# Kernel tuning notes

Hardware: AMD Instinct MI355X
Metric: run time of the kernel (lower is better)

## Reference

```python
import jax, jax.numpy as jnp
import numpy as np

ENC_DIM = 1024
DEC_DIM = 1024
BATCH = 32
SRC_LEN = 2048


def setup_inputs() -> dict:
    key = jax.random.key(0)
    k1, k2, k3, k4, k5 = jax.random.split(key, 5)
    hidden = jax.random.normal(k1, (BATCH, DEC_DIM), dtype=jnp.float32)
    encoder_outputs = jax.random.normal(k2, (SRC_LEN, BATCH, ENC_DIM), dtype=jnp.float32)
    # nn.Linear(enc+dec, dec): weight [dec, enc+dec], bias [dec]
    fan_in = ENC_DIM + DEC_DIM
    bound = 1.0 / np.sqrt(fan_in)
    attn_w = jax.random.uniform(k3, (DEC_DIM, fan_in), dtype=jnp.float32, minval=-bound, maxval=bound)
    attn_b = jax.random.uniform(k4, (DEC_DIM,), dtype=jnp.float32, minval=-bound, maxval=bound)
    # self.v = nn.Parameter(torch.rand(dec)) -> uniform [0,1)
    v = jax.random.uniform(k5, (DEC_DIM,), dtype=jnp.float32)
    return {"hidden": hidden, "encoder_outputs": encoder_outputs,
            "attn_w": attn_w, "attn_b": attn_b, "v": v}


def reference(hidden, encoder_outputs, attn_w, attn_b, v):
    src_len, batch, _ = encoder_outputs.shape
    # hidden.repeat(src_len,1,1): [src_len, batch, dec]
    h = jnp.broadcast_to(hidden[None, :, :], (src_len, batch, hidden.shape[-1]))
    x = jnp.concatenate([h, encoder_outputs], axis=2)  # [S, B, enc+dec]
    energy = jnp.tanh(jnp.einsum('sbf,df->sbd', x, attn_w) + attn_b)  # [S, B, dec]
    # v-weighted reduction over dec dim -> scores [B, S]
    scores = jnp.einsum('sbd,d->bs', energy, v)
    return jax.nn.softmax(scores, axis=1)
```

## Files before the change

kernel.cpp:

```cpp
#include <hip/hip_runtime.h>
#include <hip/hip_bf16.h>

typedef __bf16 bf16x8 __attribute__((ext_vector_type(8)));
typedef __bf16 bf16x4 __attribute__((ext_vector_type(4)));
typedef float f32x4 __attribute__((ext_vector_type(4)));

#define S_LEN 2048
#define BATCH 32
#define DIM   1024
#define FAN   (2*DIM)

__device__ __forceinline__ unsigned short f2bf(float f) {
    union { float f; unsigned u; } x; x.f = f;
    unsigned r = x.u + 0x7FFFu + ((x.u >> 16) & 1u);
    return (unsigned short)(r >> 16);
}

__device__ __forceinline__ float fast_tanh(float x) {
    float e = __expf(2.0f * x);
    return 1.0f - 2.0f / (e + 1.0f);
}

__device__ __forceinline__ int swz(int row, int col) {
    return row * 128 + (col ^ ((row & 7) << 4));
}

__device__ __forceinline__ void gload16(const void* g, void* l) {
    __builtin_amdgcn_global_load_lds((const __attribute__((address_space(1))) void*)g,
                                     (__attribute__((address_space(3))) void*)l, 16, 0, 0);
}

__global__ __launch_bounds__(256) void k_prep(const float* __restrict__ enc,
                                              unsigned short* __restrict__ encbf,
                                              const float* __restrict__ attn_w,
                                              unsigned short* __restrict__ w2bf,
                                              const float* __restrict__ hidden,
                                              const float* __restrict__ attn_b,
                                              float* __restrict__ hw) {
    const int bid = blockIdx.x, tid = threadIdx.x;
    if (bid < 4096) {
        const size_t stride = (size_t)4096 * 256;
        const size_t n8 = (size_t)S_LEN * BATCH * DIM / 8;
        for (size_t i = (size_t)bid * 256 + tid; i < n8; i += stride) {
            float4 a = ((const float4*)enc)[2 * i];
            float4 b = ((const float4*)enc)[2 * i + 1];
            bf16x8 o;
            o[0] = (__bf16)a.x; o[1] = (__bf16)a.y; o[2] = (__bf16)a.z; o[3] = (__bf16)a.w;
            o[4] = (__bf16)b.x; o[5] = (__bf16)b.y; o[6] = (__bf16)b.z; o[7] = (__bf16)b.w;
            ((bf16x8*)encbf)[i] = o;
        }
    } else if (bid < 5120) {
        const int t = (bid - 4096) * 256 + tid;
        const int n  = t >> 8;
        const int k4 = (t & 255) * 4;
        float4 w = *(const float4*)(attn_w + (size_t)n * FAN + DIM + k4);
        ushort4 o;
        o.x = f2bf(w.x); o.y = f2bf(w.y); o.z = f2bf(w.z); o.w = f2bf(w.w);
        *(ushort4*)(w2bf + (size_t)n * DIM + k4) = o;
    } else {
        const int d = bid - 5120;
        const int lane = tid & 63, w = tid >> 6;
        const float* wrow = attn_w + (size_t)d * FAN + lane * 4;
        float4 wv[4];
        #pragma unroll
        for (int c = 0; c < 4; ++c) wv[c] = *(const float4*)(wrow + c * 256);
        const float bd = attn_b[d];
        #pragma unroll
        for (int bb = 0; bb < 8; ++bb) {
            const int b = w * 8 + bb;
            const float* hrow = hidden + (size_t)b * DIM + lane * 4;
            float s = 0.f;
            #pragma unroll
            for (int c = 0; c < 4; ++c) {
                float4 h = *(const float4*)(hrow + c * 256);
                s += wv[c].x*h.x + wv[c].y*h.y + wv[c].z*h.z + wv[c].w*h.w;
            }
            #pragma unroll
            for (int o = 32; o; o >>= 1) s += __shfl_xor(s, o);
            if (lane == 0) hw[(size_t)b * DIM + d] = s + bd;
        }
    }
}

__global__ __launch_bounds__(256, 4) void k_main(const unsigned short* __restrict__ encbf,
                                                 const unsigned short* __restrict__ w2bf,
                                                 const float* __restrict__ hw,
                                                 const float* __restrict__ vvec,
                                                 float* __restrict__ partials) {
    __shared__ unsigned char Asm[128 * 128];
    __shared__ unsigned char Bsm[128 * 128];
    const int tid = threadIdx.x;

    const int x  = blockIdx.x & 7;
    const int ii = blockIdx.x >> 3;
    const int nb = ii & 7;
    const int mb = ((ii >> 3) << 3) | x;
    const int m0 = mb * 128, n0 = nb * 128;
    const int lane = tid & 63, wid = tid >> 6;
    const int wr = wid >> 1, wc = wid & 1;

    const int row8 = lane >> 3, colx = (lane & 7) ^ row8;
    const unsigned short* asrc[4];
    const unsigned short* bsrc[4];
    #pragma unroll
    for (int p = 0; p < 4; ++p) {
        const int c = wid * 4 + p;
        asrc[p] = encbf + (size_t)(m0 + 8 * c + row8) * DIM + colx * 8;
        bsrc[p] = w2bf  + (size_t)(n0 + 8 * c + row8) * DIM + colx * 8;
    }

    f32x4 acc[4][4];
    #pragma unroll
    for (int i2 = 0; i2 < 4; ++i2)
        #pragma unroll
        for (int j = 0; j < 4; ++j) acc[i2][j] = (f32x4){0.f, 0.f, 0.f, 0.f};

    #pragma unroll 1
    for (int t = 0; t < 16; ++t) {
        __syncthreads();
        #pragma unroll
        for (int p = 0; p < 4; ++p) {
            gload16(asrc[p] + t * 64, (void*)&Asm[(wid * 4 + p) * 1024]);
            gload16(bsrc[p] + t * 64, (void*)&Bsm[(wid * 4 + p) * 1024]);
        }
        __syncthreads();

        const int lrow = lane & 15;
        const int kbyte0 = (lane >> 4) * 16;
        #pragma unroll
        for (int kk = 0; kk < 2; ++kk) {
            const int kbyte = kbyte0 + kk * 64;
            bf16x8 af[4], bfr[4];
            #pragma unroll
            for (int i2 = 0; i2 < 4; ++i2)
                af[i2] = *(const bf16x8*)(&Asm[swz(wr * 64 + i2 * 16 + lrow, kbyte)]);
            #pragma unroll
            for (int j = 0; j < 4; ++j)
                bfr[j] = *(const bf16x8*)(&Bsm[swz(wc * 64 + j * 16 + lrow, kbyte)]);
            #pragma unroll
            for (int i2 = 0; i2 < 4; ++i2)
                #pragma unroll
                for (int j = 0; j < 4; ++j)
                    acc[i2][j] = __builtin_amdgcn_mfma_f32_16x16x32_bf16(af[i2], bfr[j], acc[i2][j], 0, 0, 0);
        }
    }

    const int colg = lane & 15, rowg = lane >> 4;
    #pragma unroll
    for (int i2 = 0; i2 < 4; ++i2) {
        #pragma unroll
        for (int r = 0; r < 4; ++r) {
            const int m = m0 + wr * 64 + i2 * 16 + rowg * 4 + r;
            const float* hwrow = hw + (size_t)(m & 31) * DIM + n0 + wc * 64;
            const float* vrow  = vvec + n0 + wc * 64;
            float sumv = 0.f;
            #pragma unroll
            for (int j = 0; j < 4; ++j) {
                const int nl = j * 16 + colg;
                float pre = acc[i2][j][r] + hwrow[nl];
                sumv += vrow[nl] * fast_tanh(pre);
            }
            sumv += __shfl_xor(sumv, 1);
            sumv += __shfl_xor(sumv, 2);
            sumv += __shfl_xor(sumv, 4);
            sumv += __shfl_xor(sumv, 8);
            if (colg == 0) partials[(size_t)m * 16 + nb * 2 + wc] = sumv;
        }
    }
}

__global__ __launch_bounds__(256) void k_main_f32(const float* __restrict__ enc,
                                                  const unsigned short* __restrict__ w2bf,
                                                  const float* __restrict__ hw,
                                                  const float* __restrict__ vvec,
                                                  float* __restrict__ partials) {
    __shared__ unsigned char Asm[128 * 128];
    __shared__ unsigned char Bsm[2][128 * 128];
    const int tid = threadIdx.x;
    const int x  = blockIdx.x & 7;
    const int ii = blockIdx.x >> 3;
    const int nb = ii & 7;
    const int mb = ((ii >> 3) << 3) | x;
    const int m0 = mb * 128, n0 = nb * 128;
    const int lane = tid & 63, wid = tid >> 6;
    const int wr = wid >> 1, wc = wid & 1;
    const int ar = tid >> 4, ac = tid & 15;
    const float* aptr = enc + (size_t)(m0 + ar) * DIM + ac * 4;
    const int row8 = lane >> 3, colx = (lane & 7) ^ row8;
    const unsigned short* bsrc[4];
    #pragma unroll
    for (int p = 0; p < 4; ++p)
        bsrc[p] = w2bf + (size_t)(n0 + 8 * (wid * 4 + p) + row8) * DIM + colx * 8;

    f32x4 acc[4][4];
    #pragma unroll
    for (int i2 = 0; i2 < 4; ++i2)
        #pragma unroll
        for (int j = 0; j < 4; ++j) acc[i2][j] = (f32x4){0.f, 0.f, 0.f, 0.f};

    float4 areg[8];
    #pragma unroll
    for (int p = 0; p < 8; ++p) areg[p] = *(const float4*)(aptr + p * 16 * DIM);
    #pragma unroll
    for (int p = 0; p < 4; ++p)
        gload16(bsrc[p], (void*)&Bsm[0][(wid * 4 + p) * 1024]);

    #pragma unroll 1
    for (int t = 0; t < 16; ++t) {
        asm volatile("s_waitcnt lgkmcnt(0)" ::: "memory");
        __builtin_amdgcn_s_barrier();
        #pragma unroll
        for (int p = 0; p < 8; ++p) {
            bf16x4 c;
            c[0] = (__bf16)areg[p].x; c[1] = (__bf16)areg[p].y;
            c[2] = (__bf16)areg[p].z; c[3] = (__bf16)areg[p].w;
            *(bf16x4*)(&Asm[swz(ar + p * 16, ac * 8)]) = c;
        }
        if (t + 1 < 16) {
            const int ko = (t + 1) * 64;
            #pragma unroll
            for (int p = 0; p < 8; ++p) areg[p] = *(const float4*)(aptr + ko + p * 16 * DIM);
            #pragma unroll
            for (int p = 0; p < 4; ++p)
                gload16(bsrc[p] + (size_t)(t + 1) * 64,
                        (void*)&Bsm[(t + 1) & 1][(wid * 4 + p) * 1024]);
            asm volatile("s_waitcnt vmcnt(12)" ::: "memory");
        } else {
            asm volatile("s_waitcnt vmcnt(0)" ::: "memory");
        }
        asm volatile("s_waitcnt lgkmcnt(0)" ::: "memory");
        __builtin_amdgcn_s_barrier();

        const unsigned char* bbase = &Bsm[t & 1][0];
        const int lrow = lane & 15;
        const int kbyte0 = (lane >> 4) * 16;
        #pragma unroll
        for (int kk = 0; kk < 2; ++kk) {
            const int kbyte = kbyte0 + kk * 64;
            bf16x8 af[4], bfr[4];
            #pragma unroll
            for (int i2 = 0; i2 < 4; ++i2)
                af[i2] = *(const bf16x8*)(&Asm[swz(wr * 64 + i2 * 16 + lrow, kbyte)]);
            #pragma unroll
            for (int j = 0; j < 4; ++j)
                bfr[j] = *(const bf16x8*)(&bbase[swz(wc * 64 + j * 16 + lrow, kbyte)]);
            #pragma unroll
            for (int i2 = 0; i2 < 4; ++i2)
                #pragma unroll
                for (int j = 0; j < 4; ++j)
                    acc[i2][j] = __builtin_amdgcn_mfma_f32_16x16x32_bf16(af[i2], bfr[j], acc[i2][j], 0, 0, 0);
        }
    }

    const int colg = lane & 15, rowg = lane >> 4;
    #pragma unroll
    for (int i2 = 0; i2 < 4; ++i2) {
        #pragma unroll
        for (int r = 0; r < 4; ++r) {
            const int m = m0 + wr * 64 + i2 * 16 + rowg * 4 + r;
            const float* hwrow = hw + (size_t)(m & 31) * DIM + n0 + wc * 64;
            const float* vrow  = vvec + n0 + wc * 64;
            float sumv = 0.f;
            #pragma unroll
            for (int j = 0; j < 4; ++j) {
                const int nl = j * 16 + colg;
                float pre = acc[i2][j][r] + hwrow[nl];
                sumv += vrow[nl] * fast_tanh(pre);
            }
            sumv += __shfl_xor(sumv, 1);
            sumv += __shfl_xor(sumv, 2);
            sumv += __shfl_xor(sumv, 4);
            sumv += __shfl_xor(sumv, 8);
            if (colg == 0) partials[(size_t)m * 16 + nb * 2 + wc] = sumv;
        }
    }
}

__global__ __launch_bounds__(1024) void k_softmax(const float* __restrict__ partials,
                                                  float* __restrict__ out) {
    const int b = blockIdx.x;
    const int tid = threadIdx.x;
    __shared__ float redm[16], reds[16];
    float loc[2];
    float mx = -1e30f;
    #pragma unroll
    for (int i = 0; i < 2; ++i) {
        const int s = tid + i * 1024;
        const float4* p = (const float4*)(partials + ((size_t)s * 32 + b) * 16);
        float4 p0 = p[0], p1 = p[1], p2 = p[2], p3 = p[3];
        float v = ((p0.x + p0.y) + (p0.z + p0.w)) + ((p1.x + p1.y) + (p1.z + p1.w))
                + ((p2.x + p2.y) + (p2.z + p2.w)) + ((p3.x + p3.y) + (p3.z + p3.w));
        loc[i] = v; mx = fmaxf(mx, v);
    }
    #pragma unroll
    for (int o = 32; o; o >>= 1) mx = fmaxf(mx, __shfl_xor(mx, o));
    const int wid2 = tid >> 6, lane = tid & 63;
    if (lane == 0) redm[wid2] = mx;
    __syncthreads();
    mx = redm[0];
    #pragma unroll
    for (int w = 1; w < 16; ++w) mx = fmaxf(mx, redm[w]);
    float sum = 0.f;
    #pragma unroll
    for (int i = 0; i < 2; ++i) { float e = __expf(loc[i] - mx); loc[i] = e; sum += e; }
    #pragma unroll
    for (int o = 32; o; o >>= 1) sum += __shfl_xor(sum, o);
    if (lane == 0) reds[wid2] = sum;
    __syncthreads();
    sum = 0.f;
    #pragma unroll
    for (int w = 0; w < 16; ++w) sum += reds[w];
    const float rs = 1.0f / sum;
    #pragma unroll
    for (int i = 0; i < 2; ++i) out[(size_t)b * S_LEN + tid + i * 1024] = loc[i] * rs;
}

extern "C" void kernel_launch(void* const* d_in, const int* in_sizes, int n_in,
                              void* d_out, int out_size, void* d_ws, size_t ws_size,
                              hipStream_t stream) {
    const float* hidden = (const float*)d_in[0];
    const float* enc    = (const float*)d_in[1];
    const float* attn_w = (const float*)d_in[2];
    const float* attn_b = (const float*)d_in[3];
    const float* v      = (const float*)d_in[4];
    float* out = (float*)d_out;

    char* ws = (char*)d_ws;
    float*          hw       = (float*)ws;
    unsigned short* w2bf     = (unsigned short*)(ws + (128u << 10));
    float*          partials = (float*)(ws + (128u << 10) + (2u << 20));
    unsigned short* encbf    = (unsigned short*)(ws + (128u << 10) + (6u << 20));
    const size_t NEED = (128u << 10) + (6u << 20) + ((size_t)S_LEN * BATCH * DIM * 2);

    if (ws_size >= NEED) {
        hipLaunchKernelGGL(k_prep, dim3(6144), dim3(256), 0, stream,
                           enc, encbf, attn_w, w2bf, hidden, attn_b, hw);
        hipLaunchKernelGGL(k_main, dim3(4096), dim3(256), 0, stream, encbf, w2bf, hw, v, partials);
    } else {
        hipLaunchKernelGGL(k_prep, dim3(6144), dim3(256), 0, stream,
                           enc, (unsigned short*)w2bf , attn_w, w2bf, hidden, attn_b, hw);
        hipLaunchKernelGGL(k_main_f32, dim3(4096), dim3(256), 0, stream, enc, w2bf, hw, v, partials);
    }
    hipLaunchKernelGGL(k_softmax, dim3(32), dim3(1024), 0, stream, partials, out);
}
```

Measured before the change: 244.1 us.

## Replace 128x128 GEMM with 256x256 eight-wave ping-pong pipelined kernel

The main bf16 GEMM kernel is replaced by a 512-thread kernel computing 256x256 output tiles with double-buffered LDS in quadrants. Global loads for future k-steps are issued inside eight interleaved compute phases, with barriers and setprio around the MFMA bursts, so memory traffic overlaps matrix math. Larger tiles halve the operand reloads per output and cut the block count to 1024. The cost is 128KB of LDS per block and heavier register pressure, which limits occupancy to about one or two blocks per CU.

Measured after the change: 264.4 us. +8.3%, slower.

```diff
diff --git a/kernel.cpp b/kernel.cpp
--- a/kernel.cpp
+++ b/kernel.cpp
@@ -82,91 +82,137 @@
     }
 }
 
-__global__ __launch_bounds__(256, 4) void k_main(const unsigned short* __restrict__ encbf,
-                                                 const unsigned short* __restrict__ w2bf,
-                                                 const float* __restrict__ hw,
-                                                 const float* __restrict__ vvec,
-                                                 float* __restrict__ partials) {
-    __shared__ unsigned char Asm[128 * 128];
-    __shared__ unsigned char Bsm[128 * 128];
+#define ASLOT(PAR,HH) (((PAR)*2+(HH)) << 14)
+
+#define STAGE_A(tt, HH, PAR) do {                                                    \
+    gload16(aSb[HH][0] + (tt) * 64, (void*)&Asm[ASLOT(PAR,HH) + ((wid*2+0) << 10)]); \
+    gload16(aSb[HH][1] + (tt) * 64, (void*)&Asm[ASLOT(PAR,HH) + ((wid*2+1) << 10)]); \
+  } while (0)
+
+#define STAGE_B(tt, HH, PAR) do {                                                    \
+    gload16(bSb[HH][0] + (tt) * 64, (void*)&Bsm[ASLOT(PAR,HH) + ((wid*2+0) << 10)]); \
+    gload16(bSb[HH][1] + (tt) * 64, (void*)&Bsm[ASLOT(PAR,HH) + ((wid*2+1) << 10)]); \
+  } while (0)
+
+#define PHASE(PAR, MQ, NQ, LA, LB, STAGE_STMT, VMCNT_STMT)                           \
+  {                                                                                  \
+    if (LA) {                                                                        \
+      _Pragma("unroll") for (int i2 = 0; i2 < 4; ++i2)                               \
+      _Pragma("unroll") for (int kk = 0; kk < 2; ++kk)                               \
+        afr[i2][kk] = *(const bf16x8*)(&Asm[ASLOT(PAR,MQ) +                          \
+                         swz(wr * 64 + i2 * 16 + lrow, kk * 64 + khb)]);             \
+    }                                                                                \
+    if (LB) {                                                                        \
+      _Pragma("unroll") for (int j = 0; j < 2; ++j)                                  \
+      _Pragma("unroll") for (int kk = 0; kk < 2; ++kk)                               \
+        bfr[j][kk] = *(const bf16x8*)(&Bsm[ASLOT(PAR,NQ) +                           \
+                         swz(wc * 32 + j * 16 + lrow, kk * 64 + khb)]);              \
+    }                                                                                \
+    STAGE_STMT;                                                                      \
+    VMCNT_STMT;                                                                      \
+    __builtin_amdgcn_s_barrier();                                                    \
+    asm volatile("s_waitcnt lgkmcnt(0)" ::: "memory");                               \
+    __builtin_amdgcn_sched_barrier(0);                                               \
+    __builtin_amdgcn_s_setprio(1);                                                   \
+    _Pragma("unroll") for (int i2 = 0; i2 < 4; ++i2)                                 \
+    _Pragma("unroll") for (int j = 0; j < 2; ++j)                                    \
+    _Pragma("unroll") for (int kk = 0; kk < 2; ++kk)                                 \
+      acc[MQ][NQ][i2][j] = __builtin_amdgcn_mfma_f32_16x16x32_bf16(                  \
+          afr[i2][kk], bfr[j][kk], acc[MQ][NQ][i2][j], 0, 0, 0);                     \
+    __builtin_amdgcn_s_setprio(0);                                                   \
+    __builtin_amdgcn_sched_barrier(0);                                               \
+    __builtin_amdgcn_s_barrier();                                                    \
+  }
+
+__global__ __launch_bounds__(512, 2) void k_main8(const unsigned short* __restrict__ encbf,
+                                                  const unsigned short* __restrict__ w2bf,
+                                                  const float* __restrict__ hw,
+                                                  const float* __restrict__ vvec,
+                                                  float* __restrict__ partials) {
+    __shared__ unsigned char Asm[4 * 16384];
+    __shared__ unsigned char Bsm[4 * 16384];
     const int tid = threadIdx.x;
 
     const int x  = blockIdx.x & 7;
     const int ii = blockIdx.x >> 3;
-    const int nb = ii & 7;
-    const int mb = ((ii >> 3) << 3) | x;
-    const int m0 = mb * 128, n0 = nb * 128;
+    const int nb = ii & 3;
+    const int mb = (ii >> 2) * 8 + x;
+    const int m0 = mb * 256, n0 = nb * 256;
     const int lane = tid & 63, wid = tid >> 6;
-    const int wr = wid >> 1, wc = wid & 1;
+    const int wr = wid >> 2, wc = wid & 3;
+    const int lrow = lane & 15, khb = (lane >> 4) * 16;
 
     const int row8 = lane >> 3, colx = (lane & 7) ^ row8;
-    const unsigned short* asrc[4];
-    const unsigned short* bsrc[4];
-    #pragma unroll
-    for (int p = 0; p < 4; ++p) {
-        const int c = wid * 4 + p;
-        asrc[p] = encbf + (size_t)(m0 + 8 * c + row8) * DIM + colx * 8;
-        bsrc[p] = w2bf  + (size_t)(n0 + 8 * c + row8) * DIM + colx * 8;
-    }
-
-    f32x4 acc[4][4];
-    #pragma unroll
-    for (int i2 = 0; i2 < 4; ++i2)
-        #pragma unroll
-        for (int j = 0; j < 4; ++j) acc[i2][j] = (f32x4){0.f, 0.f, 0.f, 0.f};
+    const unsigned short* aSb[2][2];
+    const unsigned short* bSb[2][2];
+    #pragma unroll
+    for (int h = 0; h < 2; ++h)
+        #pragma unroll
+        for (int q = 0; q < 2; ++q) {
+            aSb[h][q] = encbf + (size_t)(m0 + h * 128 + 16 * wid + 8 * q + row8) * DIM + colx * 8;
+            bSb[h][q] = w2bf  + (size_t)(n0 + h * 128 + 16 * wid + 8 * q + row8) * DIM + colx * 8;
+        }
+
+    f32x4 acc[2][2][4][2];
+    #pragma unroll
+    for (int a = 0; a < 2; ++a)
+        #pragma unroll
+        for (int b = 0; b < 2; ++b)
+            #pragma unroll
+            for (int c = 0; c < 4; ++c)
+                #pragma unroll
+                for (int d = 0; d < 2; ++d) acc[a][b][c][d] = (f32x4){0.f, 0.f, 0.f, 0.f};
+
+    bf16x8 afr[4][2], bfr[2][2];
+
+    STAGE_A(0, 0, 0);
+    STAGE_A(0, 1, 0);
+    STAGE_B(0, 0, 0);
+    STAGE_B(0, 1, 0);
+    STAGE_A(1, 0, 1);
+    STAGE_B(1, 1, 1);
+    asm volatile("s_waitcnt vmcnt(4)" ::: "memory");
+    __builtin_amdgcn_s_barrier();
 
     #pragma unroll 1
-    for (int t = 0; t < 16; ++t) {
-        __syncthreads();
-        #pragma unroll
-        for (int p = 0; p < 4; ++p) {
-            gload16(asrc[p] + t * 64, (void*)&Asm[(wid * 4 + p) * 1024]);
-            gload16(bsrc[p] + t * 64, (void*)&Bsm[(wid * 4 + p) * 1024]);
-        }
-        __syncthreads();
-
-        const int lrow = lane & 15;
-        const int kbyte0 = (lane >> 4) * 16;
-        #pragma unroll
-        for (int kk = 0; kk < 2; ++kk) {
-            const int kbyte = kbyte0 + kk * 64;
-            bf16x8 af[4], bfr[4];
-            #pragma unroll
-            for (int i2 = 0; i2 < 4; ++i2)
-                af[i2] = *(const bf16x8*)(&Asm[swz(wr * 64 + i2 * 16 + lrow, kbyte)]);
-            #pragma unroll
-            for (int j = 0; j < 4; ++j)
-                bfr[j] = *(const bf16x8*)(&Bsm[swz(wc * 64 + j * 16 + lrow, kbyte)]);
-            #pragma unroll
-            for (int i2 = 0; i2 < 4; ++i2)
+    for (int t = 0; t < 16; t += 2) {
+        PHASE(0, 0, 0, 1, 1, STAGE_A(t + 1, 1, 1), (void)0)
+        PHASE(0, 0, 1, 0, 1, STAGE_B(t + 1, 0, 1), (void)0)
+        PHASE(0, 1, 1, 1, 0, if (t + 2 < 16) STAGE_A(t + 2, 0, 0), (void)0)
+        PHASE(0, 1, 0, 0, 1, if (t + 2 < 16) STAGE_B(t + 2, 1, 0),
+              if (t + 2 < 16) { asm volatile("s_waitcnt vmcnt(4)" ::: "memory"); }
+              else            { asm volatile("s_waitcnt vmcnt(0)" ::: "memory"); })
+        PHASE(1, 0, 0, 1, 1, if (t + 2 < 16) STAGE_A(t + 2, 1, 0), (void)0)
+        PHASE(1, 0, 1, 0, 1, if (t + 2 < 16) STAGE_B(t + 2, 0, 0), (void)0)
+        PHASE(1, 1, 1, 1, 0, if (t + 3 < 16) STAGE_A(t + 3, 0, 1), (void)0)
+        PHASE(1, 1, 0, 0, 1, if (t + 3 < 16) STAGE_B(t + 3, 1, 1),
+              asm volatile("s_waitcnt vmcnt(4)" ::: "memory"))
+    }
+
+    const int colg = lane & 15, rowg = lane >> 4;
+    #pragma unroll
+    for (int mq = 0; mq < 2; ++mq)
+        #pragma unroll
+        for (int i2 = 0; i2 < 4; ++i2)
+            #pragma unroll
+            for (int r = 0; r < 4; ++r) {
+                const int m = m0 + mq * 128 + wr * 64 + i2 * 16 + rowg * 4 + r;
+                const float* hwrow = hw + (size_t)(m & 31) * DIM;
+                float sumv = 0.f;
                 #pragma unroll
-                for (int j = 0; j < 4; ++j)
-                    acc[i2][j] = __builtin_amdgcn_mfma_f32_16x16x32_bf16(af[i2], bfr[j], acc[i2][j], 0, 0, 0);
-        }
-    }
-
-    const int colg = lane & 15, rowg = lane >> 4;
-    #pragma unroll
-    for (int i2 = 0; i2 < 4; ++i2) {
-        #pragma unroll
-        for (int r = 0; r < 4; ++r) {
-            const int m = m0 + wr * 64 + i2 * 16 + rowg * 4 + r;
-            const float* hwrow = hw + (size_t)(m & 31) * DIM + n0 + wc * 64;
-            const float* vrow  = vvec + n0 + wc * 64;
-            float sumv = 0.f;
-            #pragma unroll
-            for (int j = 0; j < 4; ++j) {
-                const int nl = j * 16 + colg;
-                float pre = acc[i2][j][r] + hwrow[nl];
-                sumv += vrow[nl] * fast_tanh(pre);
+                for (int nq = 0; nq < 2; ++nq)
+                    #pragma unroll
+                    for (int j = 0; j < 2; ++j) {
+                        const int n = n0 + nq * 128 + wc * 32 + j * 16 + colg;
+                        float pre = acc[mq][nq][i2][j][r] + hwrow[n];
+                        sumv += vvec[n] * fast_tanh(pre);
+                    }
+                sumv += __shfl_xor(sumv, 1);
+                sumv += __shfl_xor(sumv, 2);
+                sumv += __shfl_xor(sumv, 4);
+                sumv += __shfl_xor(sumv, 8);
+                if (colg == 0) partials[(size_t)m * 16 + nb * 4 + wc] = sumv;
             }
-            sumv += __shfl_xor(sumv, 1);
-            sumv += __shfl_xor(sumv, 2);
-            sumv += __shfl_xor(sumv, 4);
-            sumv += __shfl_xor(sumv, 8);
-            if (colg == 0) partials[(size_t)m * 16 + nb * 2 + wc] = sumv;
-        }
-    }
 }
 
 __global__ __launch_bounds__(256) void k_main_f32(const float* __restrict__ enc,
@@ -174,8 +220,8 @@
                                                   const float* __restrict__ hw,
                                                   const float* __restrict__ vvec,
                                                   float* __restrict__ partials) {
-    __shared__ unsigned char Asm[128 * 128];
-    __shared__ unsigned char Bsm[2][128 * 128];
+    __shared__ unsigned char AsmL[128 * 128];
+    __shared__ unsigned char BsmL[2][128 * 128];
     const int tid = threadIdx.x;
     const int x  = blockIdx.x & 7;
     const int ii = blockIdx.x >> 3;
@@ -203,7 +249,7 @@
     for (int p = 0; p < 8; ++p) areg[p] = *(const float4*)(aptr + p * 16 * DIM);
     #pragma unroll
     for (int p = 0; p < 4; ++p)
-        gload16(bsrc[p], (void*)&Bsm[0][(wid * 4 + p) * 1024]);
+        gload16(bsrc[p], (void*)&BsmL[0][(wid * 4 + p) * 1024]);
 
     #pragma unroll 1
     for (int t = 0; t < 16; ++t) {
@@ -214,7 +260,7 @@
             bf16x4 c;
             c[0] = (__bf16)areg[p].x; c[1] = (__bf16)areg[p].y;
             c[2] = (__bf16)areg[p].z; c[3] = (__bf16)areg[p].w;
-            *(bf16x4*)(&Asm[swz(ar + p * 16, ac * 8)]) = c;
+            *(bf16x4*)(&AsmL[swz(ar + p * 16, ac * 8)]) = c;
         }
         if (t + 1 < 16) {
             const int ko = (t + 1) * 64;
@@ -223,7 +269,7 @@
             #pragma unroll
             for (int p = 0; p < 4; ++p)
                 gload16(bsrc[p] + (size_t)(t + 1) * 64,
-                        (void*)&Bsm[(t + 1) & 1][(wid * 4 + p) * 1024]);
+                        (void*)&BsmL[(t + 1) & 1][(wid * 4 + p) * 1024]);
             asm volatile("s_waitcnt vmcnt(12)" ::: "memory");
         } else {
             asm volatile("s_waitcnt vmcnt(0)" ::: "memory");
@@ -231,30 +277,30 @@
         asm volatile("s_waitcnt lgkmcnt(0)" ::: "memory");
         __builtin_amdgcn_s_barrier();
 
-        const unsigned char* bbase = &Bsm[t & 1][0];
+        const unsigned char* bbase = &BsmL[t & 1][0];
         const int lrow = lane & 15;
         const int kbyte0 = (lane >> 4) * 16;
         #pragma unroll
         for (int kk = 0; kk < 2; ++kk) {
             const int kbyte = kbyte0 + kk * 64;
-            bf16x8 af[4], bfr[4];
+            bf16x8 af[4], bfr2[4];
             #pragma unroll
             for (int i2 = 0; i2 < 4; ++i2)
-                af[i2] = *(const bf16x8*)(&Asm[swz(wr * 64 + i2 * 16 + lrow, kbyte)]);
+                af[i2] = *(const bf16x8*)(&AsmL[swz(wr * 64 + i2 * 16 + lrow, kbyte)]);
             #pragma unroll
             for (int j = 0; j < 4; ++j)
-                bfr[j] = *(const bf16x8*)(&bbase[swz(wc * 64 + j * 16 + lrow, kbyte)]);
+                bfr2[j] = *(const bf16x8*)(&bbase[swz(wc * 64 + j * 16 + lrow, kbyte)]);
             #pragma unroll
             for (int i2 = 0; i2 < 4; ++i2)
                 #pragma unroll
                 for (int j = 0; j < 4; ++j)
-                    acc[i2][j] = __builtin_amdgcn_mfma_f32_16x16x32_bf16(af[i2], bfr[j], acc[i2][j], 0, 0, 0);
+                    acc[i2][j] = __builtin_amdgcn_mfma_f32_16x16x32_bf16(af[i2], bfr2[j], acc[i2][j], 0, 0, 0);
         }
     }
 
     const int colg = lane & 15, rowg = lane >> 4;
     #pragma unroll
-    for (int i2 = 0; i2 < 4; ++i2) {
+    for (int i2 = 0; i2 < 4; ++i2)
         #pragma unroll
         for (int r = 0; r < 4; ++r) {
             const int m = m0 + wr * 64 + i2 * 16 + rowg * 4 + r;
@@ -273,7 +319,6 @@
             sumv += __shfl_xor(sumv, 8);
             if (colg == 0) partials[(size_t)m * 16 + nb * 2 + wc] = sumv;
         }
-    }
 }
 
 __global__ __launch_bounds__(1024) void k_softmax(const float* __restrict__ partials,
@@ -333,12 +378,12 @@
     const size_t NEED = (128u << 10) + (6u << 20) + ((size_t)S_LEN * BATCH * DIM * 2);
 
     if (ws_size >= NEED) {
-        hipLaunchKernelGGL(k_prep, dim3(6144), dim3(256), 0, stream,
+        hipLaunchKernelGGL(k_prep,  dim3(6144), dim3(256), 0, stream,
                            enc, encbf, attn_w, w2bf, hidden, attn_b, hw);
-        hipLaunchKernelGGL(k_main, dim3(4096), dim3(256), 0, stream, encbf, w2bf, hw, v, partials);
+        hipLaunchKernelGGL(k_main8, dim3(1024), dim3(512), 0, stream, encbf, w2bf, hw, v, partials);
     } else {
-        hipLaunchKernelGGL(k_prep, dim3(6144), dim3(256), 0, stream,
-                           enc, (unsigned short*)w2bf , attn_w, w2bf, hidden, attn_b, hw);
+        hipLaunchKernelGGL(k_prep,  dim3(6144), dim3(256), 0, stream,
+                           enc, (unsigned short*)w2bf, attn_w, w2bf, hidden, attn_b, hw);
         hipLaunchKernelGGL(k_main_f32, dim3(4096), dim3(256), 0, stream, enc, w2bf, hw, v, partials);
     }
     hipLaunchKernelGGL(k_softmax, dim3(32), dim3(1024), 0, stream, partials, out);
```
